# Optimization experiments

Measured on AMD Instinct MI355X. Metric: run time of the kernel, lower is better.

## Reference

```python
import jax, jax.numpy as jnp
import numpy as np

SIGMA = 1.0  # isotropic Gaussian bandwidth (init kwarg)


def setup_inputs() -> dict:
    key = jax.random.key(0)
    X = jax.random.normal(key, (16384, 64), dtype=jnp.float32)
    return {"X": X}


def reference(X):
    # pairwise squared distances: ||x_i||^2 - 2 x_i.x_j + ||x_j||^2
    sumX2 = jnp.sum(X * X, axis=1, keepdims=True)          # [n, 1]
    D2 = sumX2 - 2.0 * (X @ X.T) + sumX2.T                  # [n, n]
    D2 = jnp.maximum(D2, 0.0)
    K = jnp.exp(-D2 / (2.0 * SIGMA ** 2))
    return K
```

## Files before the change

kernel.cpp:

```cpp
#include <hip/hip_runtime.h>
#include <stdint.h>


typedef __attribute__((ext_vector_type(8))) short  s16x8;
typedef __attribute__((ext_vector_type(4))) float  f32x4;
typedef __attribute__((ext_vector_type(4))) unsigned short u16x4;

#define DDIM 64
#define JT 8
#define LOG2E      1.4426950408889634f
#define HALF_LOG2E 0.7213475204444817f

__device__ inline unsigned short bf16_rne(float x) {
  uint32_t u = __builtin_bit_cast(uint32_t, x);
  uint32_t r = (u + 0x7fffu + ((u >> 16) & 1u));
  return (unsigned short)(r >> 16);
}
__device__ inline float bf16_to_f32(unsigned short h) {
  return __builtin_bit_cast(float, (uint32_t)h << 16);
}

__global__ __launch_bounds__(256) void k_cvt(const float* __restrict__ X,
                                             unsigned short* __restrict__ Xb) {
  int g = blockIdx.x * 256 + threadIdx.x;
  f32x4 v = reinterpret_cast<const f32x4*>(X)[g];
  u16x4 h;
  h[0] = bf16_rne(v[0]); h[1] = bf16_rne(v[1]);
  h[2] = bf16_rne(v[2]); h[3] = bf16_rne(v[3]);
  reinterpret_cast<u16x4*>(Xb)[g] = h;
}

__global__ __launch_bounds__(256) void k_norm(const unsigned short* __restrict__ Xb,
                                              float* __restrict__ nrm) {
  int row = blockIdx.x * 256 + threadIdx.x;
  const s16x8* p = reinterpret_cast<const s16x8*>(Xb + (size_t)row * DDIM);
  float s = 0.f;
#pragma unroll
  for (int k = 0; k < 8; ++k) {
    s16x8 h = p[k];
#pragma unroll
    for (int e = 0; e < 8; ++e) {
      float f = bf16_to_f32((unsigned short)h[e]);
      s += f * f;
    }
  }
  nrm[row] = -HALF_LOG2E * s;
}

__global__ __launch_bounds__(512, 3) void gauss_main(
    const unsigned short* __restrict__ Xb, const float* __restrict__ nrm,
    float* __restrict__ K, int n) {
  const int lane = threadIdx.x & 63;
  const int wid  = threadIdx.x >> 6;
  const int wr = wid >> 2;
  const int wc = wid & 3;
  const int l15 = lane & 15;
  const int lq  = lane >> 4;

  const int i0    = blockIdx.x * 128 + wr * 64;
  const int jbase = blockIdx.y * (128 * JT);
  const int jw    = wc * 32;

  s16x8 a[4][2];
  float hA[4];
#pragma unroll
  for (int mi = 0; mi < 4; ++mi) {
    const int row = i0 + mi * 16 + l15;
#pragma unroll
    for (int ks = 0; ks < 2; ++ks)
      a[mi][ks] = *reinterpret_cast<const s16x8*>(
          Xb + (size_t)row * DDIM + ks * 32 + lq * 8);
    hA[mi] = nrm[row];
  }

  s16x8 b[3][2][2];
  float nb[3];
#define ISSUE_B(slot, jt_)                                                     \
  do {                                                                         \
    const int j0_ = jbase + (jt_) * 128 + jw;                                  \
    _Pragma("unroll") for (int ni = 0; ni < 2; ++ni) {                         \
      const int row_ = j0_ + ni * 16 + l15;                                    \
      _Pragma("unroll") for (int ks = 0; ks < 2; ++ks)                         \
        b[slot][ni][ks] = *reinterpret_cast<const s16x8*>(                     \
            Xb + (size_t)row_ * DDIM + ks * 32 + lq * 8);                      \
    }                                                                          \
    nb[slot] = nrm[j0_ + (lane & 31)];                                         \
  } while (0)

  ISSUE_B(0, 0);
  ISSUE_B(1, 1);
  ISSUE_B(2, 2);

#pragma unroll
  for (int jt = 0; jt < JT; ++jt) {
    const int slot = jt % 3;
    const int j0 = jbase + jt * 128 + jw;

    float hcol[2][4];
#pragma unroll
    for (int ni = 0; ni < 2; ++ni)
#pragma unroll
      for (int r = 0; r < 4; ++r)
        hcol[ni][r] = __shfl(nb[slot], ni * 16 + lq * 4 + r);

    f32x4 acc[4][2] = {};
#pragma unroll
    for (int ks = 0; ks < 2; ++ks)
#pragma unroll
      for (int mi = 0; mi < 4; ++mi)
#pragma unroll
        for (int ni = 0; ni < 2; ++ni)
          acc[mi][ni] = __builtin_amdgcn_mfma_f32_16x16x32_bf16(
              b[slot][ni][ks], a[mi][ks], acc[mi][ni], 0, 0, 0);

    if (jt + 3 < JT) ISSUE_B(slot, jt + 3);
    __builtin_amdgcn_sched_barrier(0x1 | 0x2 | 0x4 | 0x8);

#pragma unroll
    for (int mi = 0; mi < 4; ++mi) {
      const int rg = i0 + mi * 16 + l15;
      float* rowp = K + (size_t)rg * n;
#pragma unroll
      for (int ni = 0; ni < 2; ++ni) {
        const int c0 = j0 + ni * 16 + lq * 4;
        f32x4 v;
#pragma unroll
        for (int r = 0; r < 4; ++r) {
          float arg = fminf(hA[mi] + hcol[ni][r] + LOG2E * acc[mi][ni][r], 0.0f);
          float e = exp2f(arg);
          v[r] = (rg == c0 + r) ? 1.0f : e;
        }
        *reinterpret_cast<f32x4*>(rowp + c0) = v;
      }
    }
  }
#undef ISSUE_B
}

__device__ inline short cvt1(float x, float& sq) {
  uint32_t u = __builtin_bit_cast(uint32_t, x);
  uint32_t r = (u + 0x7fffu + ((u >> 16) & 1u)) & 0xffff0000u;
  float hf = __builtin_bit_cast(float, r);
  sq += hf * hf;
  return (short)(r >> 16);
}
__device__ inline void issue_row(const float* __restrict__ X, int row, int lq,
                                 f32x4 r[4]) {
  const f32x4* p = reinterpret_cast<const f32x4*>(X + (size_t)row * DDIM + lq * 8);
  const f32x4* q = reinterpret_cast<const f32x4*>(X + (size_t)row * DDIM + 32 + lq * 8);
  r[0] = p[0]; r[1] = p[1]; r[2] = q[0]; r[3] = q[1];
}
__device__ inline void cvt_row(const f32x4 r[4], s16x8 h[2], float& hnorm) {
  float s = 0.f;
#pragma unroll
  for (int ks = 0; ks < 2; ++ks) {
    s16x8 hh;
    hh[0] = cvt1(r[2*ks][0], s);   hh[1] = cvt1(r[2*ks][1], s);
    hh[2] = cvt1(r[2*ks][2], s);   hh[3] = cvt1(r[2*ks][3], s);
    hh[4] = cvt1(r[2*ks+1][0], s); hh[5] = cvt1(r[2*ks+1][1], s);
    hh[6] = cvt1(r[2*ks+1][2], s); hh[7] = cvt1(r[2*ks+1][3], s);
    h[ks] = hh;
  }
  s += __shfl_xor(s, 16);
  s += __shfl_xor(s, 32);
  hnorm = -HALF_LOG2E * s;
}
__global__ __launch_bounds__(256, 2) void gauss_gram_kernel(
    const float* __restrict__ X, float* __restrict__ K, int n) {
  const int lane = threadIdx.x & 63;
  const int wid  = threadIdx.x >> 6;
  const int wr = wid >> 1, wc = wid & 1;
  const int l15 = lane & 15, lq = lane >> 4;
  const int i0 = blockIdx.x * 128 + wr * 64;
  const int jstrip = blockIdx.y * (128 * JT);
  f32x4 araw[4][4];
#pragma unroll
  for (int mi = 0; mi < 4; ++mi) issue_row(X, i0 + mi * 16 + l15, lq, araw[mi]);
  f32x4 braw[4][4];
#pragma unroll
  for (int ni = 0; ni < 4; ++ni)
    issue_row(X, jstrip + wc * 64 + ni * 16 + l15, lq, braw[ni]);
  s16x8 a[4][2]; float hA[4];
#pragma unroll
  for (int mi = 0; mi < 4; ++mi) cvt_row(araw[mi], a[mi], hA[mi]);
#pragma unroll
  for (int jt = 0; jt < JT; ++jt) {
    const int j0 = jstrip + jt * 128 + wc * 64;
    s16x8 b[4][2]; float hcol[4][4];
#pragma unroll
    for (int ni = 0; ni < 4; ++ni) {
      float hB;
      cvt_row(braw[ni], b[ni], hB);
#pragma unroll
      for (int r = 0; r < 4; ++r) hcol[ni][r] = __shfl(hB, lq * 4 + r);
    }
    if (jt + 1 < JT) {
#pragma unroll
      for (int ni = 0; ni < 4; ++ni)
        issue_row(X, jstrip + (jt + 1) * 128 + wc * 64 + ni * 16 + l15, lq, braw[ni]);
    }
    __builtin_amdgcn_sched_barrier(0x1 | 0x2 | 0x4 | 0x8);
    f32x4 acc[4][4] = {};
#pragma unroll
    for (int ks = 0; ks < 2; ++ks)
#pragma unroll
      for (int mi = 0; mi < 4; ++mi)
#pragma unroll
        for (int ni = 0; ni < 4; ++ni)
          acc[mi][ni] = __builtin_amdgcn_mfma_f32_16x16x32_bf16(
              b[ni][ks], a[mi][ks], acc[mi][ni], 0, 0, 0);
#pragma unroll
    for (int mi = 0; mi < 4; ++mi) {
      const int rg = i0 + mi * 16 + l15;
      float* rowp = K + (size_t)rg * n;
#pragma unroll
      for (int ni = 0; ni < 4; ++ni) {
        const int c0 = j0 + ni * 16 + lq * 4;
        f32x4 v;
#pragma unroll
        for (int r = 0; r < 4; ++r) {
          float arg = fminf(hA[mi] + hcol[ni][r] + LOG2E * acc[mi][ni][r], 0.0f);
          float e = exp2f(arg);
          v[r] = (rg == c0 + r) ? 1.0f : e;
        }
        *reinterpret_cast<f32x4*>(rowp + c0) = v;
      }
    }
  }
}

extern "C" void kernel_launch(void* const* d_in, const int* in_sizes, int n_in,
                              void* d_out, int out_size, void* d_ws, size_t ws_size,
                              hipStream_t stream) {
  (void)n_in; (void)out_size;
  const float* X = (const float*)d_in[0];
  float* K = (float*)d_out;
  const int n = in_sizes[0] / DDIM;
  const size_t need = (size_t)n * DDIM * 2 + (size_t)n * 4;
  if (ws_size >= need) {
    unsigned short* Xb = (unsigned short*)d_ws;
    float* nrm = (float*)((char*)d_ws + (size_t)n * DDIM * 2);
    k_cvt<<<dim3(n * DDIM / 4 / 256), 256, 0, stream>>>(X, Xb);
    k_norm<<<dim3(n / 256), 256, 0, stream>>>(Xb, nrm);
    dim3 grid(n / 128, n / (128 * JT));
    gauss_main<<<grid, 512, 0, stream>>>(Xb, nrm, K, n);
  } else {
    dim3 grid(n / 128, n / (128 * JT));
    gauss_gram_kernel<<<grid, 256, 0, stream>>>(X, K, n);
  }
}
```

Measured before the change: 269.3 us.

## Stage output tiles through per-wave LDS for coalesced row stores

Each wave now writes its exp results into a padded per-wave shared-memory tile and then streams it out so that consecutive lanes store contiguous row segments. Before this, each 16-byte store went to a different row. The main kernel also moves to 256-thread blocks with a 64-column step, a two-slot prefetch of B tiles, column norms loaded as vectors instead of shuffled, and the diagonal check applied only on tiles that touch the diagonal. The aim is better write coalescing on the 1 GB output, which bounds this kernel. In exchange it adds LDS traffic, and the removed clamp to zero could let values slightly exceed 1 through rounding.

```diff
diff --git a/kernel.cpp b/kernel.cpp
--- a/kernel.cpp
+++ b/kernel.cpp
@@ -8,6 +8,7 @@
 
 #define DDIM 64
 #define JT 8
+#define LROW 36
 #define LOG2E      1.4426950408889634f
 #define HALF_LOG2E 0.7213475204444817f
 
@@ -47,61 +48,58 @@
   nrm[row] = -HALF_LOG2E * s;
 }
 
-__global__ __launch_bounds__(512, 3) void gauss_main(
+__global__ __launch_bounds__(256, 3) void gauss_main(
     const unsigned short* __restrict__ Xb, const float* __restrict__ nrm,
     float* __restrict__ K, int n) {
   const int lane = threadIdx.x & 63;
   const int wid  = threadIdx.x >> 6;
-  const int wr = wid >> 2;
-  const int wc = wid & 3;
+  const int wr = wid >> 1;
+  const int wc = wid & 1;
   const int l15 = lane & 15;
   const int lq  = lane >> 4;
-
-  const int i0    = blockIdx.x * 128 + wr * 64;
-  const int jbase = blockIdx.y * (128 * JT);
-  const int jw    = wc * 32;
-
-  s16x8 a[4][2];
-  float hA[4];
+  const int r8  = lane >> 3;
+  const int e8  = lane & 7;
+
+  __shared__ float tbuf[4][64 * LROW];
+  float* buf = tbuf[wid];
+
+  const int i0     = blockIdx.x * 128 + wr * 64;
+  const int jstrip = blockIdx.y * (64 * JT);
+
+  s16x8 a[4][2]; float hA[4];
 #pragma unroll
   for (int mi = 0; mi < 4; ++mi) {
     const int row = i0 + mi * 16 + l15;
-#pragma unroll
-    for (int ks = 0; ks < 2; ++ks)
-      a[mi][ks] = *reinterpret_cast<const s16x8*>(
-          Xb + (size_t)row * DDIM + ks * 32 + lq * 8);
+    a[mi][0] = *reinterpret_cast<const s16x8*>(Xb + (size_t)row * DDIM + lq * 8);
+    a[mi][1] = *reinterpret_cast<const s16x8*>(Xb + (size_t)row * DDIM + 32 + lq * 8);
     hA[mi] = nrm[row];
   }
 
-  s16x8 b[3][2][2];
-  float nb[3];
+  s16x8 b[2][2][2];
+  f32x4 hc[2][2];
 #define ISSUE_B(slot, jt_)                                                     \
   do {                                                                         \
-    const int j0_ = jbase + (jt_) * 128 + jw;                                  \
+    const int j0_ = jstrip + (jt_) * 64 + wc * 32;                             \
     _Pragma("unroll") for (int ni = 0; ni < 2; ++ni) {                         \
       const int row_ = j0_ + ni * 16 + l15;                                    \
-      _Pragma("unroll") for (int ks = 0; ks < 2; ++ks)                         \
-        b[slot][ni][ks] = *reinterpret_cast<const s16x8*>(                     \
-            Xb + (size_t)row_ * DDIM + ks * 32 + lq * 8);                      \
+      b[slot][ni][0] = *reinterpret_cast<const s16x8*>(                        \
+          Xb + (size_t)row_ * DDIM + lq * 8);                                  \
+      b[slot][ni][1] = *reinterpret_cast<const s16x8*>(                        \
+          Xb + (size_t)row_ * DDIM + 32 + lq * 8);                             \
+      hc[slot][ni] = *reinterpret_cast<const f32x4*>(                          \
+          nrm + j0_ + ni * 16 + lq * 4);                                       \
     }                                                                          \
-    nb[slot] = nrm[j0_ + (lane & 31)];                                         \
   } while (0)
 
   ISSUE_B(0, 0);
-  ISSUE_B(1, 1);
-  ISSUE_B(2, 2);
 
 #pragma unroll
   for (int jt = 0; jt < JT; ++jt) {
-    const int slot = jt % 3;
-    const int j0 = jbase + jt * 128 + jw;
-
-    float hcol[2][4];
-#pragma unroll
-    for (int ni = 0; ni < 2; ++ni)
-#pragma unroll
-      for (int r = 0; r < 4; ++r)
-        hcol[ni][r] = __shfl(nb[slot], ni * 16 + lq * 4 + r);
+    const int slot = jt & 1;
+    const int j0 = jstrip + jt * 64 + wc * 32;
+
+    if (jt + 1 < JT) ISSUE_B(slot ^ 1, jt + 1);
+    __builtin_amdgcn_sched_barrier(0x1 | 0x2 | 0x4 | 0x8);
 
     f32x4 acc[4][2] = {};
 #pragma unroll
@@ -113,25 +111,36 @@
           acc[mi][ni] = __builtin_amdgcn_mfma_f32_16x16x32_bf16(
               b[slot][ni][ks], a[mi][ks], acc[mi][ni], 0, 0, 0);
 
-    if (jt + 3 < JT) ISSUE_B(slot, jt + 3);
-    __builtin_amdgcn_sched_barrier(0x1 | 0x2 | 0x4 | 0x8);
+    const bool diag = (i0 < j0 + 32) && (j0 < i0 + 64);
 
 #pragma unroll
     for (int mi = 0; mi < 4; ++mi) {
       const int rg = i0 + mi * 16 + l15;
-      float* rowp = K + (size_t)rg * n;
 #pragma unroll
       for (int ni = 0; ni < 2; ++ni) {
         const int c0 = j0 + ni * 16 + lq * 4;
         f32x4 v;
-#pragma unroll
-        for (int r = 0; r < 4; ++r) {
-          float arg = fminf(hA[mi] + hcol[ni][r] + LOG2E * acc[mi][ni][r], 0.0f);
-          float e = exp2f(arg);
-          v[r] = (rg == c0 + r) ? 1.0f : e;
+        if (diag) {
+#pragma unroll
+          for (int r = 0; r < 4; ++r) {
+            float e = exp2f(hA[mi] + hc[slot][ni][r] + LOG2E * acc[mi][ni][r]);
+            v[r] = (rg == c0 + r) ? 1.0f : e;
+          }
+        } else {
+#pragma unroll
+          for (int r = 0; r < 4; ++r)
+            v[r] = exp2f(hA[mi] + hc[slot][ni][r] + LOG2E * acc[mi][ni][r]);
         }
-        *reinterpret_cast<f32x4*>(rowp + c0) = v;
+        *reinterpret_cast<f32x4*>(
+            buf + (mi * 16 + l15) * LROW + ni * 16 + lq * 4) = v;
       }
+    }
+
+#pragma unroll
+    for (int g = 0; g < 8; ++g) {
+      const int row = g * 8 + r8;
+      f32x4 t = *reinterpret_cast<const f32x4*>(buf + row * LROW + e8 * 4);
+      *reinterpret_cast<f32x4*>(K + (size_t)(i0 + row) * n + j0 + e8 * 4) = t;
     }
   }
 #undef ISSUE_B
@@ -171,6 +180,9 @@
   const int wid  = threadIdx.x >> 6;
   const int wr = wid >> 1, wc = wid & 1;
   const int l15 = lane & 15, lq = lane >> 4;
+  const int e16 = lane & 15, r4 = lane >> 4;
+  __shared__ float tbuf[4][64 * 68];
+  float* buf = tbuf[wid];
   const int i0 = blockIdx.x * 128 + wr * 64;
   const int jstrip = blockIdx.y * (128 * JT);
   f32x4 araw[4][4];
@@ -212,7 +224,6 @@
 #pragma unroll
     for (int mi = 0; mi < 4; ++mi) {
       const int rg = i0 + mi * 16 + l15;
-      float* rowp = K + (size_t)rg * n;
 #pragma unroll
       for (int ni = 0; ni < 4; ++ni) {
         const int c0 = j0 + ni * 16 + lq * 4;
@@ -223,8 +234,14 @@
           float e = exp2f(arg);
           v[r] = (rg == c0 + r) ? 1.0f : e;
         }
-        *reinterpret_cast<f32x4*>(rowp + c0) = v;
+        *reinterpret_cast<f32x4*>(buf + (mi * 16 + l15) * 68 + ni * 16 + lq * 4) = v;
       }
+    }
+#pragma unroll
+    for (int g = 0; g < 16; ++g) {
+      const int row = g * 4 + r4;
+      f32x4 t = *reinterpret_cast<const f32x4*>(buf + row * 68 + e16 * 4);
+      *reinterpret_cast<f32x4*>(K + (size_t)(i0 + row) * n + j0 + e16 * 4) = t;
     }
   }
 }
@@ -242,8 +259,8 @@
     float* nrm = (float*)((char*)d_ws + (size_t)n * DDIM * 2);
     k_cvt<<<dim3(n * DDIM / 4 / 256), 256, 0, stream>>>(X, Xb);
     k_norm<<<dim3(n / 256), 256, 0, stream>>>(Xb, nrm);
-    dim3 grid(n / 128, n / (128 * JT));
-    gauss_main<<<grid, 512, 0, stream>>>(Xb, nrm, K, n);
+    dim3 grid(n / 128, n / (64 * JT));
+    gauss_main<<<grid, 256, 0, stream>>>(Xb, nrm, K, n);
   } else {
     dim3 grid(n / 128, n / (128 * JT));
     gauss_gram_kernel<<<grid, 256, 0, stream>>>(X, K, n);
```

Measured after the change: 229.1 us. 1.18x faster.
